# Kernel optimization log

Measured on AMD Instinct MI355X. Metric: run time of the kernel, lower is better.

## Reference

```python
import jax, jax.numpy as jnp
import numpy as np

P = 256          # patches per (batch*time) element
EPS = 1e-6
WEIGHT_SIM = 1.0
WEIGHT_GRAM = 10.0


def setup_inputs() -> dict:
    key = jax.random.key(0)
    k1, k2 = jax.random.split(key)
    N, D = 16384, 768  # N = bt * P with bt = 64
    inp = jax.random.normal(k1, (N, D), dtype=jnp.float32)
    tgt = jax.random.normal(k2, (N, D), dtype=jnp.float32)
    return {"input": inp, "target": tgt}


def _l2n(x):
    return x / jnp.sqrt(jnp.sum(x * x, axis=-1, keepdims=True)).clip(1e-12)


def reference(input, target):
    target = jax.lax.stop_gradient(target)
    N, D = input.shape
    bt = N // P

    input_n = _l2n(input)
    target_n = _l2n(target)

    input_view = input.reshape(bt, P, D)
    target_view = target.reshape(bt, P, D)
    in_n = input_n.reshape(bt, P, D)
    tg_n = target_n.reshape(bt, P, D)

    # gram of normalized targets; its row-mean gives tf
    gram_gt = jnp.einsum('bpd,bqd->bpq', tg_n, tg_n)           # [bt, P, P]
    tf = 1.0 / (gram_gt.mean(axis=-1) + EPS)                    # [bt, P]

    # cross_sim.mean(dim=-1) == all_patches @ mean(all_patches): O(N*d) not O(N^2*d)
    mean_patch = target_n.mean(axis=0)                          # [D]
    cross_mean = target_n @ mean_patch                          # [N]
    idf = 1.0 / (cross_mean.reshape(bt, P) + EPS)               # [bt, P]

    weights = tf * idf
    weights = weights / (weights.sum(axis=1, keepdims=True) + EPS)

    patch_loss = jnp.mean((input_view - target_view) ** 2, axis=-1)  # [bt, P]
    sim_loss = jnp.mean(jnp.sum(weights * patch_loss, axis=1))

    gram_pred = jnp.einsum('bpd,bqd->bpq', in_n, in_n)          # [bt, P, P]
    diff2 = (gram_pred - gram_gt) ** 2
    pair_w = weights[:, :, None] * weights[:, None, :]          # [bt, P, P]
    gram_loss = jnp.mean(jnp.sum(pair_w * diff2, axis=(1, 2)))

    return WEIGHT_SIM * sim_loss + WEIGHT_GRAM * gram_loss
```

## Files before the change

kernel.cpp:

```cpp
#include <hip/hip_runtime.h>
#include <hip/hip_bf16.h>

#define NROWS 16384
#define DIM   768
#define PP    256
#define BT    64
#define EPSF  1e-6f
#define GKC   32
#define NTILE 10
#define NGRAM (BT * NTILE)
#define SPITCH 776
#define RPW    4
#define NWG_N  (NROWS / RPW)

typedef short          bf16x8 __attribute__((ext_vector_type(8)));
typedef float          f32x4  __attribute__((ext_vector_type(4)));
typedef unsigned short us8    __attribute__((ext_vector_type(8)));

__device__ __forceinline__ unsigned short f2bf(float x) {
    __hip_bfloat16 h = __float2bfloat16(x);
    return *reinterpret_cast<unsigned short*>(&h);
}

template<int PRE>
__global__ __launch_bounds__(256, 8) void k_norms(const float* __restrict__ in,
                                                  const float* __restrict__ tg,
                                                  float* __restrict__ inv_in,
                                                  float* __restrict__ inv_tg,
                                                  float* __restrict__ ploss,
                                                  unsigned short* __restrict__ in_n,
                                                  unsigned short* __restrict__ tg_n,
                                                  float* __restrict__ psum) {
    __shared__ __align__(16) float S[RPW][SPITCH];
    const int r   = threadIdx.x >> 6;
    const int c   = threadIdx.x & 63;
    const int row = blockIdx.x * RPW + r;
    const float4* ip = (const float4*)(in + (size_t)row * DIM);
    const float4* tp = (const float4*)(tg + (size_t)row * DIM);
    float4 a[3], t[3];
#pragma unroll
    for (int k = 0; k < 3; ++k) { a[k] = ip[c + 64 * k]; t[k] = tp[c + 64 * k]; }
    float si = 0.f, st = 0.f, sd = 0.f;
#pragma unroll
    for (int k = 0; k < 3; ++k) {
        si += a[k].x*a[k].x + a[k].y*a[k].y + a[k].z*a[k].z + a[k].w*a[k].w;
        st += t[k].x*t[k].x + t[k].y*t[k].y + t[k].z*t[k].z + t[k].w*t[k].w;
        float dx = a[k].x-t[k].x, dy = a[k].y-t[k].y, dz = a[k].z-t[k].z, dw = a[k].w-t[k].w;
        sd += dx*dx + dy*dy + dz*dz + dw*dw;
    }
#pragma unroll
    for (int o = 32; o; o >>= 1) {
        si += __shfl_xor(si, o); st += __shfl_xor(st, o); sd += __shfl_xor(sd, o);
    }
    float ii = 1.f / fmaxf(sqrtf(si), 1e-12f);
    float it = 1.f / fmaxf(sqrtf(st), 1e-12f);
    if (c == 0) { inv_in[row] = ii; inv_tg[row] = it; ploss[row] = sd * (1.f / DIM); }

#pragma unroll
    for (int k = 0; k < 3; ++k) {
        float4 u = t[k];
        u.x *= it; u.y *= it; u.z *= it; u.w *= it;
        *(float4*)&S[r][4 * c + 256 * k] = u;
    }

    if constexpr (PRE != 0) {
#pragma unroll
        for (int k = 0; k < 3; ++k) {
            unsigned long long ua, ut;
            unsigned short x0 = f2bf(a[k].x * ii), x1 = f2bf(a[k].y * ii);
            unsigned short x2 = f2bf(a[k].z * ii), x3 = f2bf(a[k].w * ii);
            unsigned short y0 = f2bf(t[k].x * it), y1 = f2bf(t[k].y * it);
            unsigned short y2 = f2bf(t[k].z * it), y3 = f2bf(t[k].w * it);
            ua = (unsigned long long)x0 | ((unsigned long long)x1 << 16)
               | ((unsigned long long)x2 << 32) | ((unsigned long long)x3 << 48);
            ut = (unsigned long long)y0 | ((unsigned long long)y1 << 16)
               | ((unsigned long long)y2 << 32) | ((unsigned long long)y3 << 48);
            *(unsigned long long*)(in_n + (size_t)row * DIM + 4 * c + 256 * k) = ua;
            *(unsigned long long*)(tg_n + (size_t)row * DIM + 4 * c + 256 * k) = ut;
        }
    }

    __syncthreads();
#pragma unroll
    for (int q = 0; q < 3; ++q) {
        int d = threadIdx.x + 256 * q;
        float s = 0.f;
#pragma unroll
        for (int rr = 0; rr < RPW; ++rr) s += S[rr][d];
        psum[(size_t)blockIdx.x * DIM + d] = s;
    }
}


__global__ __launch_bounds__(256) void k_bsum2(const float* __restrict__ psum,
                                               float* __restrict__ bsum) {
    int b = blockIdx.x, d = blockIdx.y * 256 + threadIdx.x;
    float s = 0.f;
#pragma unroll 8
    for (int i = 0; i < 64; ++i)
        s += psum[(size_t)(b * 64 + i) * DIM + d];
    bsum[b * DIM + d] = s;
}

__global__ __launch_bounds__(256) void k_gmean(const float* __restrict__ bsum,
                                               float* __restrict__ va) {
    int d = blockIdx.x * 256 + threadIdx.x;
    float g = 0.f;
    for (int b = 0; b < BT; ++b) g += bsum[b * DIM + d];
    va[d] = g * (1.f / NROWS);
}

__global__ __launch_bounds__(256) void k_wdots(const float* __restrict__ tg,
                                               const float* __restrict__ inv_tg,
                                               const float* __restrict__ bsum,
                                               const float* __restrict__ va,
                                               float* __restrict__ wraw) {
    int wave = threadIdx.x >> 6, lane = threadIdx.x & 63;
    int gw = blockIdx.x * 4 + wave;
#pragma unroll
    for (int rr = 0; rr < 4; ++rr) {
        int row = gw * 4 + rr;
        int b   = row >> 8;
        const float4* t4 = (const float4*)(tg + (size_t)row * DIM);
        const float4* b4 = (const float4*)(bsum + b * DIM);
        const float4* a4 = (const float4*)va;
        float db = 0.f, da = 0.f;
#pragma unroll
        for (int v = 0; v < 3; ++v) {
            float4 t = t4[lane + 64 * v];
            float4 x = b4[lane + 64 * v];
            float4 y = a4[lane + 64 * v];
            db += t.x * x.x + t.y * x.y + t.z * x.z + t.w * x.w;
            da += t.x * y.x + t.y * y.y + t.z * y.z + t.w * y.w;
        }
#pragma unroll
        for (int o = 32; o; o >>= 1) { db += __shfl_xor(db, o); da += __shfl_xor(da, o); }
        if (lane == 0) {
            float itg = inv_tg[row];
            db *= itg; da *= itg;
            wraw[row] = (1.f / (db * (1.f / PP) + EPSF)) * (1.f / (da + EPSF));
        }
    }
}

__global__ __launch_bounds__(256) void k_wfinal(const float* __restrict__ wraw,
                                                const float* __restrict__ ploss,
                                                float* __restrict__ weights,
                                                float* __restrict__ simpart) {
    __shared__ float red[256];
    int b = blockIdx.x, p = threadIdx.x, row = b * PP + p;
    float w = wraw[row];
    red[p] = w; __syncthreads();
    for (int s = 128; s; s >>= 1) { if (p < s) red[p] += red[p + s]; __syncthreads(); }
    float wn = w / (red[0] + EPSF);
    weights[row] = wn;
    __syncthreads();
    red[p] = wn * ploss[row]; __syncthreads();
    for (int s = 128; s; s >>= 1) { if (p < s) red[p] += red[p + s]; __syncthreads(); }
    if (p == 0) simpart[b] = red[0];
}

__global__ __launch_bounds__(256, 3) void k_gram(const unsigned short* __restrict__ in_n,
                                                 const unsigned short* __restrict__ tg_n,
                                                 const float* __restrict__ weights,
                                                 float* __restrict__ grampart) {
    __shared__ __align__(16) unsigned short L[2][4][64 * GKC];
    __shared__ float red[256];

    const int wg  = blockIdx.x;
    const int xcd = wg & 7, j = wg >> 3;
    const int b   = xcd * 8 + j / NTILE;
    const int t   = j % NTILE;
    int ti, tj;
    if (t < 4)      { ti = 0; tj = t; }
    else if (t < 7) { ti = 1; tj = t - 3; }
    else if (t < 9) { ti = 2; tj = t - 5; }
    else            { ti = 3; tj = 3; }
    const int pr = ti * 64, qc = tj * 64;
    const bool diag = (ti == tj);
    const float factor = diag ? 1.f : 2.f;
    const int bP = b * PP;

    const int tid = threadIdx.x, lane = tid & 63, wave = tid >> 6;

    const unsigned short* smat = (wave & 1) ? tg_n : in_n;
    const int  srow0   = bP + ((wave < 2) ? pr : qc);
    const bool doStage = !(diag && wave >= 2);
    const int  srl = lane >> 2;
    const int  scc = lane & 3;
    const int  wcc = scc ^ (srl & 3);

    us8 sreg[4];
    auto LD = [&](int k0) {
        if (!doStage) return;
#pragma unroll
        for (int i = 0; i < 4; ++i)
            sreg[i] = *(const us8*)(smat + (size_t)(srow0 + 16 * i + srl) * DIM + k0 + scc * 8);
    };
    auto WR = [&](int cur) {
        if (!doStage) return;
#pragma unroll
        for (int i = 0; i < 4; ++i)
            *(us8*)&L[cur][wave][(16 * i + srl) * GKC + wcc * 8] = sreg[i];
    };

    const int ar0 = (wave >> 1) * 32, bc0 = (wave & 1) * 32;
    const int rl = lane & 15, kc = lane >> 4;
    const int bi_ = diag ? 0 : 2, bt_ = diag ? 1 : 3;

    f32x4 accI[2][2], accT[2][2];
#pragma unroll
    for (int m = 0; m < 2; ++m)
#pragma unroll
        for (int n = 0; n < 2; ++n) {
            f32x4 z = { 0.f, 0.f, 0.f, 0.f };
            accI[m][n] = z; accT[m][n] = z;
        }

    LD(0); WR(0);
    int cur = 0;
    const int NS = DIM / GKC;
    for (int ks = 0; ks < NS; ++ks) {
        if (ks + 1 < NS) LD((ks + 1) * GKC);
        __syncthreads();
        bf16x8 aI[2], aT[2], bI[2], bT[2];
#pragma unroll
        for (int m = 0; m < 2; ++m) {
            int row = ar0 + m * 16 + rl;
            int off = row * GKC + ((kc ^ (row & 3)) << 3);
            aI[m] = *(const bf16x8*)&L[cur][0][off];
            aT[m] = *(const bf16x8*)&L[cur][1][off];
        }
#pragma unroll
        for (int n = 0; n < 2; ++n) {
            int row = bc0 + n * 16 + rl;
            int off = row * GKC + ((kc ^ (row & 3)) << 3);
            bI[n] = *(const bf16x8*)&L[cur][bi_][off];
            bT[n] = *(const bf16x8*)&L[cur][bt_][off];
        }
#pragma unroll
        for (int m = 0; m < 2; ++m)
#pragma unroll
            for (int n = 0; n < 2; ++n) {
                accI[m][n] = __builtin_amdgcn_mfma_f32_16x16x32_bf16(aI[m], bI[n], accI[m][n], 0, 0, 0);
                accT[m][n] = __builtin_amdgcn_mfma_f32_16x16x32_bf16(aT[m], bT[n], accT[m][n], 0, 0, 0);
            }
        if (ks + 1 < NS) WR(cur ^ 1);
        cur ^= 1;
    }

    const int r4 = lane >> 4, cl = lane & 15;
    float wq[2], wp[2][4];
#pragma unroll
    for (int n = 0; n < 2; ++n) wq[n] = weights[bP + qc + bc0 + n * 16 + cl];
#pragma unroll
    for (int m = 0; m < 2; ++m)
#pragma unroll
        for (int r = 0; r < 4; ++r) wp[m][r] = weights[bP + pr + ar0 + m * 16 + r4 * 4 + r];
    float local = 0.f;
#pragma unroll
    for (int m = 0; m < 2; ++m)
#pragma unroll
        for (int n = 0; n < 2; ++n)
#pragma unroll
            for (int r = 0; r < 4; ++r) {
                float d = accI[m][n][r] - accT[m][n][r];
                local += wp[m][r] * wq[n] * d * d;
            }
    local *= factor;
    red[tid] = local; __syncthreads();
    for (int s = 128; s; s >>= 1) { if (tid < s) red[tid] += red[tid + s]; __syncthreads(); }
    if (tid == 0) grampart[wg] = red[0];
}

#define LP 40
__global__ __launch_bounds__(256) void k_gram_f32(const float* __restrict__ in,
                                                  const float* __restrict__ tg,
                                                  const float* __restrict__ inv_in,
                                                  const float* __restrict__ inv_tg,
                                                  const float* __restrict__ weights,
                                                  float* __restrict__ grampart) {
    __shared__ __align__(16) unsigned short LA0[128 * LP];
    __shared__ __align__(16) unsigned short LA1[128 * LP];
    __shared__ __align__(16) unsigned short LB0[128 * LP];
    __shared__ __align__(16) unsigned short LB1[128 * LP];
    __shared__ float red[256];

    const int wg  = blockIdx.x;
    const int xcd = wg & 7, j = wg >> 3;
    const int b   = xcd * 8 + j / 3;
    const int t3  = j % 3;
    const int pr  = (t3 == 2) ? 128 : 0;
    const int qc  = (t3 == 0) ? 0 : 128;
    const bool diag = (pr == qc);
    const float factor = diag ? 1.f : 2.f;

    const int tid  = threadIdx.x;
    const int lane = tid & 63;
    const int wave = tid >> 6;
    const int wr = (wave >> 1) * 64, wc = (wave & 1) * 64;
    const int bP = b * PP;

    const int strow = tid >> 2;
    const int skq   = tid & 3;
    const int sw    = (strow >> 3) & 3;

    const float* srcf[4] = { in, tg, in, tg };
    unsigned short* ldst[4] = { LA0, LA1, LB0, LB1 };

    size_t g[4][2];
#pragma unroll
    for (int h = 0; h < 2; ++h) {
        g[0][h] = (size_t)(bP + pr + strow + h * 64) * DIM + skq * 8;
        g[1][h] = g[0][h];
        g[2][h] = (size_t)(bP + qc + strow + h * 64) * DIM + skq * 8;
        g[3][h] = g[2][h];
    }
    float scl[4][2];
#pragma unroll
    for (int h = 0; h < 2; ++h) {
        scl[0][h] = inv_in[bP + pr + strow + h * 64];
        scl[1][h] = inv_tg[bP + pr + strow + h * 64];
        scl[2][h] = inv_in[bP + qc + strow + h * 64];
        scl[3][h] = inv_tg[bP + qc + strow + h * 64];
    }

    float4 pfa[4][2], pfb[4][2];

    auto STAGE_LOAD = [&](int k0) {
#pragma unroll
        for (int bi = 0; bi < 4; ++bi) {
            if (bi >= 2 && diag) continue;
#pragma unroll
            for (int h = 0; h < 2; ++h) {
                pfa[bi][h] = *(const float4*)(srcf[bi] + g[bi][h] + k0);
                pfb[bi][h] = *(const float4*)(srcf[bi] + g[bi][h] + k0 + 4);
            }
        }
    };
    auto STAGE_WRITE = [&]() {
#pragma unroll
        for (int bi = 0; bi < 4; ++bi) {
            if (bi >= 2 && diag) continue;
#pragma unroll
            for (int h = 0; h < 2; ++h) {
                us8 v;
                float s = scl[bi][h];
                float4 x = pfa[bi][h], y = pfb[bi][h];
                v[0] = f2bf(x.x * s); v[1] = f2bf(x.y * s);
                v[2] = f2bf(x.z * s); v[3] = f2bf(x.w * s);
                v[4] = f2bf(y.x * s); v[5] = f2bf(y.y * s);
                v[6] = f2bf(y.z * s); v[7] = f2bf(y.w * s);
                int row = strow + h * 64;
                *(us8*)&ldst[bi][row * LP + (skq ^ sw) * 8] = v;
            }
        }
    };

    const unsigned short* RB0 = diag ? LA0 : LB0;
    const unsigned short* RB1 = diag ? LA1 : LB1;

    f32x4 accI[4][4], accT[4][4];
#pragma unroll
    for (int m = 0; m < 4; ++m)
#pragma unroll
        for (int n = 0; n < 4; ++n) {
            f32x4 z = { 0.f, 0.f, 0.f, 0.f };
            accI[m][n] = z; accT[m][n] = z;
        }

    STAGE_LOAD(0);
    for (int ks = 0; ks < DIM / GKC; ++ks) {
        __syncthreads();
        STAGE_WRITE();
        __syncthreads();
        if (ks + 1 < DIM / GKC) STAGE_LOAD(GKC * (ks + 1));

        bf16x8 aI[4], aT[4], bI[4], bT[4];
#pragma unroll
        for (int m = 0; m < 4; ++m) {
            int row = wr + m * 16 + (lane & 15);
            int off = row * LP + (((lane >> 4) ^ ((row >> 3) & 3))) * 8;
            aI[m] = *(const bf16x8*)&LA0[off];
            aT[m] = *(const bf16x8*)&LA1[off];
        }
#pragma unroll
        for (int n = 0; n < 4; ++n) {
            int row = wc + n * 16 + (lane & 15);
            int off = row * LP + (((lane >> 4) ^ ((row >> 3) & 3))) * 8;
            bI[n] = *(const bf16x8*)&RB0[off];
            bT[n] = *(const bf16x8*)&RB1[off];
        }
#pragma unroll
        for (int m = 0; m < 4; ++m)
#pragma unroll
            for (int n = 0; n < 4; ++n) {
                accI[m][n] = __builtin_amdgcn_mfma_f32_16x16x32_bf16(aI[m], bI[n], accI[m][n], 0, 0, 0);
                accT[m][n] = __builtin_amdgcn_mfma_f32_16x16x32_bf16(aT[m], bT[n], accT[m][n], 0, 0, 0);
            }
    }

    const int r4 = lane >> 4, cl = lane & 15;
    float wq[4], wp[4][4];
#pragma unroll
    for (int n = 0; n < 4; ++n) wq[n] = weights[bP + qc + wc + n * 16 + cl];
#pragma unroll
    for (int m = 0; m < 4; ++m)
#pragma unroll
        for (int r = 0; r < 4; ++r) wp[m][r] = weights[bP + pr + wr + m * 16 + r4 * 4 + r];
    float local = 0.f;
#pragma unroll
    for (int m = 0; m < 4; ++m)
#pragma unroll
        for (int n = 0; n < 4; ++n)
#pragma unroll
            for (int r = 0; r < 4; ++r) {
                float d = accI[m][n][r] - accT[m][n][r];
                local += wp[m][r] * wq[n] * d * d;
            }
    local *= factor;
    red[tid] = local; __syncthreads();
    for (int s = 128; s; s >>= 1) { if (tid < s) red[tid] += red[tid + s]; __syncthreads(); }
    if (tid == 0) grampart[wg] = red[0];
}

__global__ __launch_bounds__(256) void k_final(const float* __restrict__ simpart,
                                               const float* __restrict__ grampart,
                                               int ngram,
                                               float* __restrict__ out) {
    __shared__ float red[256];
    int t = threadIdx.x;
    float v = (t < BT) ? simpart[t] : 0.f;
    float g = 0.f;
    for (int i = t; i < ngram; i += 256) g += grampart[i];
    v += 10.f * g;
    red[t] = v; __syncthreads();
    for (int s = 128; s; s >>= 1) { if (t < s) red[t] += red[t + s]; __syncthreads(); }
    if (t == 0) out[0] = red[0] * (1.f / BT);
}

extern "C" void kernel_launch(void* const* d_in, const int* in_sizes, int n_in,
                              void* d_out, int out_size, void* d_ws, size_t ws_size,
                              hipStream_t stream) {
    (void)in_sizes; (void)n_in; (void)out_size;
    const float* in = (const float*)d_in[0];
    const float* tg = (const float*)d_in[1];

    const size_t bfBytes   = (size_t)NROWS * DIM * 2;
    const size_t floatsOff = 2 * bfBytes;
    const size_t fCount    = 5 * (size_t)NROWS + (size_t)NWG_N * DIM
                           + (size_t)BT * DIM + DIM + BT + NGRAM;
    const size_t needed    = floatsOff + fCount * 4;
    const bool   pre       = ws_size >= needed;

    char* wsb = (char*)d_ws;
    unsigned short* in_n = nullptr;
    unsigned short* tg_n = nullptr;
    float* fbase;
    if (pre) {
        in_n  = (unsigned short*)wsb;
        tg_n  = (unsigned short*)(wsb + bfBytes);
        fbase = (float*)(wsb + floatsOff);
    } else {
        fbase = (float*)wsb;
    }
    float* inv_in  = fbase;
    float* inv_tg  = fbase + NROWS;
    float* ploss   = fbase + 2 * (size_t)NROWS;
    float* wraw    = fbase + 3 * (size_t)NROWS;
    float* weights = fbase + 4 * (size_t)NROWS;
    float* psum    = fbase + 5 * (size_t)NROWS;
    float* bsum    = psum + (size_t)NWG_N * DIM;
    float* va      = bsum + (size_t)BT * DIM;
    float* simpart = va + DIM;
    float* grampart= simpart + BT;

    if (pre) {
        k_norms<1><<<NWG_N, 256, 0, stream>>>(in, tg, inv_in, inv_tg, ploss, in_n, tg_n, psum);
    } else {
        k_norms<0><<<NWG_N, 256, 0, stream>>>(in, tg, inv_in, inv_tg, ploss, nullptr, nullptr, psum);
    }
    k_bsum2<<<dim3(BT, 3), 256, 0, stream>>>(psum, bsum);
    k_gmean<<<3, 256, 0, stream>>>(bsum, va);
    k_wdots<<<NROWS / 16, 256, 0, stream>>>(tg, inv_tg, bsum, va, wraw);
    k_wfinal<<<BT, 256, 0, stream>>>(wraw, ploss, weights, simpart);
    if (pre) {
        k_gram<<<NGRAM, 256, 0, stream>>>(in_n, tg_n, weights, grampart);
        k_final<<<1, 256, 0, stream>>>(simpart, grampart, NGRAM, (float*)d_out);
    } else {
        k_gram_f32<<<192, 256, 0, stream>>>(in, tg, inv_in, inv_tg, weights, grampart);
        k_final<<<1, 256, 0, stream>>>(simpart, grampart, 192, (float*)d_out);
    }
}
```

Baseline: 71.84 us.

## Drop bf16 normalized copies; gram kernel reads fp32 inputs and rescales accumulators

Removes the pass in the norms kernel that wrote bf16-normalized copies of input and target to workspace. The gram kernel now loads raw fp32 rows, converts them to bf16 while staging to LDS, and applies the per-row inverse norms to the accumulated dot products in the epilogue. This also deletes the fallback fp32 gram kernel and the workspace-size branch. It saves 2x bf16 writes and reads of the matrices, but the gram kernel now reads twice the bytes per tile across 640 workgroups with overlapping tiles, and it converts unnormalized values to bf16 before scaling.

New measurement: 72.30 us. Within noise of the previous version (+0.6%).

```diff
diff --git a/kernel.cpp b/kernel.cpp
--- a/kernel.cpp
+++ b/kernel.cpp
@@ -22,14 +22,11 @@
     return *reinterpret_cast<unsigned short*>(&h);
 }
 
-template<int PRE>
 __global__ __launch_bounds__(256, 8) void k_norms(const float* __restrict__ in,
                                                   const float* __restrict__ tg,
                                                   float* __restrict__ inv_in,
                                                   float* __restrict__ inv_tg,
                                                   float* __restrict__ ploss,
-                                                  unsigned short* __restrict__ in_n,
-                                                  unsigned short* __restrict__ tg_n,
                                                   float* __restrict__ psum) {
     __shared__ __align__(16) float S[RPW][SPITCH];
     const int r   = threadIdx.x >> 6;
@@ -62,24 +59,6 @@
         u.x *= it; u.y *= it; u.z *= it; u.w *= it;
         *(float4*)&S[r][4 * c + 256 * k] = u;
     }
-
-    if constexpr (PRE != 0) {
-#pragma unroll
-        for (int k = 0; k < 3; ++k) {
-            unsigned long long ua, ut;
-            unsigned short x0 = f2bf(a[k].x * ii), x1 = f2bf(a[k].y * ii);
-            unsigned short x2 = f2bf(a[k].z * ii), x3 = f2bf(a[k].w * ii);
-            unsigned short y0 = f2bf(t[k].x * it), y1 = f2bf(t[k].y * it);
-            unsigned short y2 = f2bf(t[k].z * it), y3 = f2bf(t[k].w * it);
-            ua = (unsigned long long)x0 | ((unsigned long long)x1 << 16)
-               | ((unsigned long long)x2 << 32) | ((unsigned long long)x3 << 48);
-            ut = (unsigned long long)y0 | ((unsigned long long)y1 << 16)
-               | ((unsigned long long)y2 << 32) | ((unsigned long long)y3 << 48);
-            *(unsigned long long*)(in_n + (size_t)row * DIM + 4 * c + 256 * k) = ua;
-            *(unsigned long long*)(tg_n + (size_t)row * DIM + 4 * c + 256 * k) = ut;
-        }
-    }
-
     __syncthreads();
 #pragma unroll
     for (int q = 0; q < 3; ++q) {
@@ -160,8 +139,10 @@
     if (p == 0) simpart[b] = red[0];
 }
 
-__global__ __launch_bounds__(256, 3) void k_gram(const unsigned short* __restrict__ in_n,
-                                                 const unsigned short* __restrict__ tg_n,
+__global__ __launch_bounds__(256, 3) void k_gram(const float* __restrict__ in,
+                                                 const float* __restrict__ tg,
+                                                 const float* __restrict__ inv_in,
+                                                 const float* __restrict__ inv_tg,
                                                  const float* __restrict__ weights,
                                                  float* __restrict__ grampart) {
     __shared__ __align__(16) unsigned short L[2][4][64 * GKC];
@@ -183,25 +164,34 @@
 
     const int tid = threadIdx.x, lane = tid & 63, wave = tid >> 6;
 
-    const unsigned short* smat = (wave & 1) ? tg_n : in_n;
+    const float* smat = (wave & 1) ? tg : in;
     const int  srow0   = bP + ((wave < 2) ? pr : qc);
     const bool doStage = !(diag && wave >= 2);
     const int  srl = lane >> 2;
     const int  scc = lane & 3;
     const int  wcc = scc ^ (srl & 3);
 
-    us8 sreg[4];
+    float4 p0[4], p1[4];
     auto LD = [&](int k0) {
         if (!doStage) return;
 #pragma unroll
-        for (int i = 0; i < 4; ++i)
-            sreg[i] = *(const us8*)(smat + (size_t)(srow0 + 16 * i + srl) * DIM + k0 + scc * 8);
+        for (int i = 0; i < 4; ++i) {
+            const float* base = smat + (size_t)(srow0 + 16 * i + srl) * DIM + k0 + scc * 8;
+            p0[i] = *(const float4*)base;
+            p1[i] = *(const float4*)(base + 4);
+        }
     };
     auto WR = [&](int cur) {
         if (!doStage) return;
 #pragma unroll
-        for (int i = 0; i < 4; ++i)
-            *(us8*)&L[cur][wave][(16 * i + srl) * GKC + wcc * 8] = sreg[i];
+        for (int i = 0; i < 4; ++i) {
+            us8 v;
+            v[0] = f2bf(p0[i].x); v[1] = f2bf(p0[i].y);
+            v[2] = f2bf(p0[i].z); v[3] = f2bf(p0[i].w);
+            v[4] = f2bf(p1[i].x); v[5] = f2bf(p1[i].y);
+            v[6] = f2bf(p1[i].z); v[7] = f2bf(p1[i].w);
+            *(us8*)&L[cur][wave][(16 * i + srl) * GKC + wcc * 8] = v;
+        }
     };
 
     const int ar0 = (wave >> 1) * 32, bc0 = (wave & 1) * 32;
@@ -250,13 +240,20 @@
     }
 
     const int r4 = lane >> 4, cl = lane & 15;
-    float wq[2], wp[2][4];
-#pragma unroll
-    for (int n = 0; n < 2; ++n) wq[n] = weights[bP + qc + bc0 + n * 16 + cl];
+    float wq[2], qI[2], qT[2];
+#pragma unroll
+    for (int n = 0; n < 2; ++n) {
+        int q = bP + qc + bc0 + n * 16 + cl;
+        wq[n] = weights[q]; qI[n] = inv_in[q]; qT[n] = inv_tg[q];
+    }
+    float wp[2][4], pI[2][4], pT[2][4];
 #pragma unroll
     for (int m = 0; m < 2; ++m)
 #pragma unroll
-        for (int r = 0; r < 4; ++r) wp[m][r] = weights[bP + pr + ar0 + m * 16 + r4 * 4 + r];
+        for (int r = 0; r < 4; ++r) {
+            int p = bP + pr + ar0 + m * 16 + r4 * 4 + r;
+            wp[m][r] = weights[p]; pI[m][r] = inv_in[p]; pT[m][r] = inv_tg[p];
+        }
     float local = 0.f;
 #pragma unroll
     for (int m = 0; m < 2; ++m)
@@ -264,158 +261,8 @@
         for (int n = 0; n < 2; ++n)
 #pragma unroll
             for (int r = 0; r < 4; ++r) {
-                float d = accI[m][n][r] - accT[m][n][r];
-                local += wp[m][r] * wq[n] * d * d;
-            }
-    local *= factor;
-    red[tid] = local; __syncthreads();
-    for (int s = 128; s; s >>= 1) { if (tid < s) red[tid] += red[tid + s]; __syncthreads(); }
-    if (tid == 0) grampart[wg] = red[0];
-}
-
-#define LP 40
-__global__ __launch_bounds__(256) void k_gram_f32(const float* __restrict__ in,
-                                                  const float* __restrict__ tg,
-                                                  const float* __restrict__ inv_in,
-                                                  const float* __restrict__ inv_tg,
-                                                  const float* __restrict__ weights,
-                                                  float* __restrict__ grampart) {
-    __shared__ __align__(16) unsigned short LA0[128 * LP];
-    __shared__ __align__(16) unsigned short LA1[128 * LP];
-    __shared__ __align__(16) unsigned short LB0[128 * LP];
-    __shared__ __align__(16) unsigned short LB1[128 * LP];
-    __shared__ float red[256];
-
-    const int wg  = blockIdx.x;
-    const int xcd = wg & 7, j = wg >> 3;
-    const int b   = xcd * 8 + j / 3;
-    const int t3  = j % 3;
-    const int pr  = (t3 == 2) ? 128 : 0;
-    const int qc  = (t3 == 0) ? 0 : 128;
-    const bool diag = (pr == qc);
-    const float factor = diag ? 1.f : 2.f;
-
-    const int tid  = threadIdx.x;
-    const int lane = tid & 63;
-    const int wave = tid >> 6;
-    const int wr = (wave >> 1) * 64, wc = (wave & 1) * 64;
-    const int bP = b * PP;
-
-    const int strow = tid >> 2;
-    const int skq   = tid & 3;
-    const int sw    = (strow >> 3) & 3;
-
-    const float* srcf[4] = { in, tg, in, tg };
-    unsigned short* ldst[4] = { LA0, LA1, LB0, LB1 };
-
-    size_t g[4][2];
-#pragma unroll
-    for (int h = 0; h < 2; ++h) {
-        g[0][h] = (size_t)(bP + pr + strow + h * 64) * DIM + skq * 8;
-        g[1][h] = g[0][h];
-        g[2][h] = (size_t)(bP + qc + strow + h * 64) * DIM + skq * 8;
-        g[3][h] = g[2][h];
-    }
-    float scl[4][2];
-#pragma unroll
-    for (int h = 0; h < 2; ++h) {
-        scl[0][h] = inv_in[bP + pr + strow + h * 64];
-        scl[1][h] = inv_tg[bP + pr + strow + h * 64];
-        scl[2][h] = inv_in[bP + qc + strow + h * 64];
-        scl[3][h] = inv_tg[bP + qc + strow + h * 64];
-    }
-
-    float4 pfa[4][2], pfb[4][2];
-
-    auto STAGE_LOAD = [&](int k0) {
-#pragma unroll
-        for (int bi = 0; bi < 4; ++bi) {
-            if (bi >= 2 && diag) continue;
-#pragma unroll
-            for (int h = 0; h < 2; ++h) {
-                pfa[bi][h] = *(const float4*)(srcf[bi] + g[bi][h] + k0);
-                pfb[bi][h] = *(const float4*)(srcf[bi] + g[bi][h] + k0 + 4);
-            }
-        }
-    };
-    auto STAGE_WRITE = [&]() {
-#pragma unroll
-        for (int bi = 0; bi < 4; ++bi) {
-            if (bi >= 2 && diag) continue;
-#pragma unroll
-            for (int h = 0; h < 2; ++h) {
-                us8 v;
-                float s = scl[bi][h];
-                float4 x = pfa[bi][h], y = pfb[bi][h];
-                v[0] = f2bf(x.x * s); v[1] = f2bf(x.y * s);
-                v[2] = f2bf(x.z * s); v[3] = f2bf(x.w * s);
-                v[4] = f2bf(y.x * s); v[5] = f2bf(y.y * s);
-                v[6] = f2bf(y.z * s); v[7] = f2bf(y.w * s);
-                int row = strow + h * 64;
-                *(us8*)&ldst[bi][row * LP + (skq ^ sw) * 8] = v;
-            }
-        }
-    };
-
-    const unsigned short* RB0 = diag ? LA0 : LB0;
-    const unsigned short* RB1 = diag ? LA1 : LB1;
-
-    f32x4 accI[4][4], accT[4][4];
-#pragma unroll
-    for (int m = 0; m < 4; ++m)
-#pragma unroll
-        for (int n = 0; n < 4; ++n) {
-            f32x4 z = { 0.f, 0.f, 0.f, 0.f };
-            accI[m][n] = z; accT[m][n] = z;
-        }
-
-    STAGE_LOAD(0);
-    for (int ks = 0; ks < DIM / GKC; ++ks) {
-        __syncthreads();
-        STAGE_WRITE();
-        __syncthreads();
-        if (ks + 1 < DIM / GKC) STAGE_LOAD(GKC * (ks + 1));
-
-        bf16x8 aI[4], aT[4], bI[4], bT[4];
-#pragma unroll
-        for (int m = 0; m < 4; ++m) {
-            int row = wr + m * 16 + (lane & 15);
-            int off = row * LP + (((lane >> 4) ^ ((row >> 3) & 3))) * 8;
-            aI[m] = *(const bf16x8*)&LA0[off];
-            aT[m] = *(const bf16x8*)&LA1[off];
-        }
-#pragma unroll
-        for (int n = 0; n < 4; ++n) {
-            int row = wc + n * 16 + (lane & 15);
-            int off = row * LP + (((lane >> 4) ^ ((row >> 3) & 3))) * 8;
-            bI[n] = *(const bf16x8*)&RB0[off];
-            bT[n] = *(const bf16x8*)&RB1[off];
-        }
-#pragma unroll
-        for (int m = 0; m < 4; ++m)
-#pragma unroll
-            for (int n = 0; n < 4; ++n) {
-                accI[m][n] = __builtin_amdgcn_mfma_f32_16x16x32_bf16(aI[m], bI[n], accI[m][n], 0, 0, 0);
-                accT[m][n] = __builtin_amdgcn_mfma_f32_16x16x32_bf16(aT[m], bT[n], accT[m][n], 0, 0, 0);
-            }
-    }
-
-    const int r4 = lane >> 4, cl = lane & 15;
-    float wq[4], wp[4][4];
-#pragma unroll
-    for (int n = 0; n < 4; ++n) wq[n] = weights[bP + qc + wc + n * 16 + cl];
-#pragma unroll
-    for (int m = 0; m < 4; ++m)
-#pragma unroll
-        for (int r = 0; r < 4; ++r) wp[m][r] = weights[bP + pr + wr + m * 16 + r4 * 4 + r];
-    float local = 0.f;
-#pragma unroll
-    for (int m = 0; m < 4; ++m)
-#pragma unroll
-        for (int n = 0; n < 4; ++n)
-#pragma unroll
-            for (int r = 0; r < 4; ++r) {
-                float d = accI[m][n][r] - accT[m][n][r];
+                float d = accI[m][n][r] * pI[m][r] * qI[n]
+                        - accT[m][n][r] * pT[m][r] * qT[n];
                 local += wp[m][r] * wq[n] * d * d;
             }
     local *= factor;
@@ -442,28 +289,11 @@
 extern "C" void kernel_launch(void* const* d_in, const int* in_sizes, int n_in,
                               void* d_out, int out_size, void* d_ws, size_t ws_size,
                               hipStream_t stream) {
-    (void)in_sizes; (void)n_in; (void)out_size;
+    (void)in_sizes; (void)n_in; (void)out_size; (void)ws_size;
     const float* in = (const float*)d_in[0];
     const float* tg = (const float*)d_in[1];
 
-    const size_t bfBytes   = (size_t)NROWS * DIM * 2;
-    const size_t floatsOff = 2 * bfBytes;
-    const size_t fCount    = 5 * (size_t)NROWS + (size_t)NWG_N * DIM
-                           + (size_t)BT * DIM + DIM + BT + NGRAM;
-    const size_t needed    = floatsOff + fCount * 4;
-    const bool   pre       = ws_size >= needed;
-
-    char* wsb = (char*)d_ws;
-    unsigned short* in_n = nullptr;
-    unsigned short* tg_n = nullptr;
-    float* fbase;
-    if (pre) {
-        in_n  = (unsigned short*)wsb;
-        tg_n  = (unsigned short*)(wsb + bfBytes);
-        fbase = (float*)(wsb + floatsOff);
-    } else {
-        fbase = (float*)wsb;
-    }
+    float* fbase   = (float*)d_ws;
     float* inv_in  = fbase;
     float* inv_tg  = fbase + NROWS;
     float* ploss   = fbase + 2 * (size_t)NROWS;
@@ -475,20 +305,11 @@
     float* simpart = va + DIM;
     float* grampart= simpart + BT;
 
-    if (pre) {
-        k_norms<1><<<NWG_N, 256, 0, stream>>>(in, tg, inv_in, inv_tg, ploss, in_n, tg_n, psum);
-    } else {
-        k_norms<0><<<NWG_N, 256, 0, stream>>>(in, tg, inv_in, inv_tg, ploss, nullptr, nullptr, psum);
-    }
+    k_norms<<<NWG_N, 256, 0, stream>>>(in, tg, inv_in, inv_tg, ploss, psum);
     k_bsum2<<<dim3(BT, 3), 256, 0, stream>>>(psum, bsum);
     k_gmean<<<3, 256, 0, stream>>>(bsum, va);
     k_wdots<<<NROWS / 16, 256, 0, stream>>>(tg, inv_tg, bsum, va, wraw);
     k_wfinal<<<BT, 256, 0, stream>>>(wraw, ploss, weights, simpart);
-    if (pre) {
-        k_gram<<<NGRAM, 256, 0, stream>>>(in_n, tg_n, weights, grampart);
-        k_final<<<1, 256, 0, stream>>>(simpart, grampart, NGRAM, (float*)d_out);
-    } else {
-        k_gram_f32<<<192, 256, 0, stream>>>(in, tg, inv_in, inv_tg, weights, grampart);
-        k_final<<<1, 256, 0, stream>>>(simpart, grampart, 192, (float*)d_out);
-    }
-}
+    k_gram<<<NGRAM, 256, 0, stream>>>(in, tg, inv_in, inv_tg, weights, grampart);
+    k_final<<<1, 256, 0, stream>>>(simpart, grampart, NGRAM, (float*)d_out);
+}
```
